# Optimization experiments

Measured on AMD Instinct MI355X. Metric: run time of the kernel, lower is better.

## Reference

```python
import jax, jax.numpy as jnp
import numpy as np

HEADS = 4
DIM_HEAD = 32
IN_CHANNELS = 256
SCALE = DIM_HEAD ** -0.5
EPS = 1e-5


def setup_inputs() -> dict:
    key = jax.random.key(0)
    ks = jax.random.split(key, 6)
    B, C, H, W = 16, IN_CHANNELS, 64, 64
    inner = HEADS * DIM_HEAD  # 128
    x = jax.random.normal(ks[0], (B, C, H, W), dtype=jnp.float32)
    # 1x1 conv weights are [out_ch, in_ch] (kernel spatial dims are 1)
    w_qkv = jax.random.normal(ks[1], (3 * inner, C), dtype=jnp.float32) * (C ** -0.5)
    w_out = jax.random.normal(ks[2], (C, inner), dtype=jnp.float32) * (inner ** -0.5)
    b_out = jax.random.normal(ks[3], (C,), dtype=jnp.float32) * 0.01
    gn_gamma = jnp.ones((C,), dtype=jnp.float32)
    gn_beta = jnp.zeros((C,), dtype=jnp.float32)
    return {"x": x, "w_qkv": w_qkv, "w_out": w_out, "b_out": b_out,
            "gn_gamma": gn_gamma, "gn_beta": gn_beta}


def reference(x, w_qkv, w_out, b_out, gn_gamma, gn_beta):
    b, c, h, w = x.shape
    n = h * w
    inner = HEADS * DIM_HEAD
    # 1x1 conv (no bias): [b, 3*inner, h, w], then chunk into q,k,v along channels
    qkv = jnp.einsum('oc,bchw->bohw', w_qkv, x)
    qkv = qkv.reshape(b, 3, HEADS, DIM_HEAD, n)  # chunk + 'b (h c) x y -> b h c (x y)'
    q, k, v = qkv[:, 0], qkv[:, 1], qkv[:, 2]    # each [b, heads, dim_head, n]
    q = jax.nn.softmax(q, axis=-2) * SCALE       # softmax over dim_head axis
    k = jax.nn.softmax(k, axis=-1)               # softmax over spatial axis
    context = jnp.einsum('bhdn,bhen->bhde', k, v)  # [b, heads, d, e]
    out = jnp.einsum('bhde,bhdn->bhen', context, q)  # [b, heads, e, n]
    out = out.reshape(b, inner, h, w)            # 'b h c (x y) -> b (h c) x y'
    # out 1x1 conv with bias
    out = jnp.einsum('oc,bchw->bohw', w_out, out) + b_out[None, :, None, None]
    # GroupNorm(num_groups=1): normalize over (C,H,W) per sample, per-channel affine
    mean = jnp.mean(out, axis=(1, 2, 3), keepdims=True)
    var = jnp.var(out, axis=(1, 2, 3), keepdims=True)
    out = (out - mean) * jax.lax.rsqrt(var + EPS)
    return out * gn_gamma[None, :, None, None] + gn_beta[None, :, None, None]
```

## Files before the change

kernel.cpp:

```cpp
#include <hip/hip_runtime.h>
#include <hip/hip_bf16.h>
#include <math.h>

#define B_SZ 16
#define C_IN 256
#define HEADS 4
#define DHEAD 32
#define INNER 128
#define QKV_CH 384
#define N_PIX 4096
#define SCALE_Q 0.17677669529663687f
#define GN_EPS 1e-5f
#define NCHK 32

typedef __attribute__((ext_vector_type(8))) short s16x8;
typedef __attribute__((ext_vector_type(4))) float f32x4;
typedef __attribute__((ext_vector_type(8))) unsigned short u16x8;
typedef __attribute__((ext_vector_type(4))) unsigned short u16x4;

#define VMCNT(n) asm volatile("s_waitcnt vmcnt(" #n ")" ::: "memory")
#define LGKMCNT0 asm volatile("s_waitcnt lgkmcnt(0)" ::: "memory")

__device__ __forceinline__ float waveSum(float v) {
#pragma unroll
  for (int off = 32; off > 0; off >>= 1) v += __shfl_down(v, off, 64);
  return v;
}
__device__ __forceinline__ unsigned short f2bf(float f) {
  unsigned int u = __builtin_bit_cast(unsigned int, f);
  unsigned int r = 0x7FFFu + ((u >> 16) & 1u);
  return (unsigned short)((u + r) >> 16);
}
__device__ __forceinline__ float bf2f(unsigned short u) {
  unsigned int x = ((unsigned int)u) << 16;
  return __builtin_bit_cast(float, x);
}

__global__ __launch_bounds__(256) void cvt_w(const float* __restrict__ wq,
                                             const float* __restrict__ wo,
                                             unsigned short* __restrict__ wqb,
                                             unsigned short* __restrict__ wob) {
  const int i = blockIdx.x * 256 + threadIdx.x;
  if (i < QKV_CH * C_IN) wqb[i] = f2bf(wq[i]);
  if (i < C_IN * INNER) wob[i] = f2bf(wo[i]);
}

__global__ __launch_bounds__(512, 4) void qkv_gemm(const unsigned short* __restrict__ A,
                                                   const float* __restrict__ X,
                                                   unsigned short* __restrict__ Out,
                                                   unsigned short* __restrict__ qsm_t) {
  const int b = blockIdx.y;
  const int n0 = blockIdx.x * 64;
  const int tid = threadIdx.x;
  const int w = tid >> 6, l = tid & 63;
  const int lr = l & 15, kg = l >> 4;
  const int wm = w >> 1, wn = w & 1;

  __shared__ char lds[65536];
  char* As = lds;
  char* Bs = lds + 49152;

  const int c_loc = ((tid >> 3) & 7) + w * 8;
  const int oct = tid & 7;
  const float* xbase = X + (size_t)b * C_IN * N_PIX + (size_t)c_loc * N_PIX + n0 + oct * 8;

  auto ISSUE_A = [&](int kc, int half) {
#pragma unroll
    for (int it = 0; it < 3; ++it) {
      const int idx = it * 512 + tid;
      const int r = idx >> 3;
      const int srcb = ((idx & 7) << 4) ^ ((r & 7) << 4);
      __builtin_amdgcn_global_load_lds(
          (const __attribute__((address_space(1))) void*)((const char*)A +
              ((size_t)(half * 192 + r) * C_IN + kc * 64) * 2 + srcb),
          (__attribute__((address_space(3))) void*)(As + half * 24576 + idx * 16), 16, 0, 0);
    }
  };

  f32x4 xr0, xr1;
  auto ISSUE_X = [&](int kc) {
    const float* xp = xbase + (size_t)(kc * 64) * N_PIX;
    xr0 = *reinterpret_cast<const f32x4*>(xp);
    xr1 = *reinterpret_cast<const f32x4*>(xp + 4);
  };

  auto WRITE_B = [&](int pb) {
#pragma unroll
    for (int j = 0; j < 8; ++j) {
      const int n = oct * 8 + j;
      const float v = (j < 4) ? xr0[j] : xr1[j - 4];
      *reinterpret_cast<unsigned short*>(
          Bs + pb * 8192 + n * 128 + ((2 * c_loc) ^ (((n ^ (n >> 3)) & 7) << 4))) = f2bf(v);
    }
  };

  f32x4 acc[2][3][2] = {};

  auto COMPUTE = [&](int kc, int half) {
    const char* Ab = As + half * 24576;
    const char* Bb = Bs + (kc & 1) * 8192;
#pragma unroll
    for (int ks = 0; ks < 2; ++ks) {
      const int kb = ks * 64 + kg * 16;
      s16x8 av[3], bv[2];
#pragma unroll
      for (int i = 0; i < 3; ++i) {
        const int r = wm * 48 + i * 16 + lr;
        av[i] = *reinterpret_cast<const s16x8*>(Ab + r * 128 + (kb ^ ((r & 7) << 4)));
      }
#pragma unroll
      for (int j = 0; j < 2; ++j) {
        const int n = wn * 32 + j * 16 + lr;
        bv[j] = *reinterpret_cast<const s16x8*>(Bb + n * 128 +
                                                (kb ^ (((n ^ (n >> 3)) & 7) << 4)));
      }
#pragma unroll
      for (int i = 0; i < 3; ++i)
#pragma unroll
        for (int j = 0; j < 2; ++j)
          acc[half][i][j] =
              __builtin_amdgcn_mfma_f32_16x16x32_bf16(av[i], bv[j], acc[half][i][j], 0, 0, 0);
    }
  };

  ISSUE_A(0, 0);
  ISSUE_X(0);
  VMCNT(0);
  WRITE_B(0);
  LGKMCNT0;
  __builtin_amdgcn_s_barrier();

  for (int kc = 0; kc < 4; ++kc) {
    ISSUE_A(kc, 1);
    if (kc < 3) {
      ISSUE_X(kc + 1);
      VMCNT(5);
    } else {
      VMCNT(3);
    }
    __builtin_amdgcn_s_barrier();
    COMPUTE(kc, 0);
    LGKMCNT0;
    __builtin_amdgcn_s_barrier();
    if (kc < 3) {
      ISSUE_A(kc + 1, 0);
      VMCNT(3);
    } else {
      VMCNT(0);
    }
    __builtin_amdgcn_s_barrier();
    if (kc < 3) WRITE_B((kc + 1) & 1);
    COMPUTE(kc, 1);
    LGKMCNT0;
    __builtin_amdgcn_s_barrier();
  }

  unsigned short* Ob = Out + (size_t)b * QKV_CH * N_PIX;
#pragma unroll
  for (int half = 0; half < 2; ++half)
#pragma unroll
    for (int i = 0; i < 3; ++i) {
      const int mt = wm * 48 + i * 16;
      if (half == 1 || mt >= 128) {
        const int mrow = half * 192 + mt + kg * 4;
#pragma unroll
        for (int j = 0; j < 2; ++j) {
          const int col = n0 + wn * 32 + j * 16 + lr;
#pragma unroll
          for (int r = 0; r < 4; ++r)
            Ob[(size_t)(mrow + r) * N_PIX + col] = f2bf(acc[half][i][j][r]);
        }
      }
    }

  float* qs = (float*)lds;
#pragma unroll
  for (int i = 0; i < 3; ++i) {
    const int mt = wm * 48 + i * 16;
    if (mt < 128) {
      const int rowb = mt + kg * 4;
#pragma unroll
      for (int j = 0; j < 2; ++j) {
        const int c_l = wn * 32 + j * 16 + lr;
        *reinterpret_cast<f32x4*>(qs + c_l * 132 + rowb) = acc[0][i][j];
      }
    }
  }
  LGKMCNT0;
  __builtin_amdgcn_s_barrier();

  if (tid < 256) {
    const int n_loc = tid & 63, h = tid >> 6;
    const float* qrow = qs + n_loc * 132 + h * 32;
    f32x4 qv[8];
#pragma unroll
    for (int c = 0; c < 8; ++c) qv[c] = *reinterpret_cast<const f32x4*>(qrow + c * 4);
    float m = qv[0][0];
#pragma unroll
    for (int c = 0; c < 8; ++c)
#pragma unroll
      for (int r = 0; r < 4; ++r) m = fmaxf(m, qv[c][r]);
    float e[32];
    float s = 0.f;
#pragma unroll
    for (int c = 0; c < 8; ++c)
#pragma unroll
      for (int r = 0; r < 4; ++r) {
        e[c * 4 + r] = __expf(qv[c][r] - m);
        s += e[c * 4 + r];
      }
    const float inv = SCALE_Q / s;
    unsigned short* ob = qsm_t + ((size_t)b * N_PIX + n0 + n_loc) * INNER + h * DHEAD;
#pragma unroll
    for (int d8 = 0; d8 < 4; ++d8) {
      u16x8 pk;
#pragma unroll
      for (int r = 0; r < 8; ++r) pk[r] = f2bf(e[d8 * 8 + r] * inv);
      *reinterpret_cast<u16x8*>(&ob[d8 * 8]) = pk;
    }
  }
}

__global__ __launch_bounds__(256) void ctx_mfma(const unsigned short* __restrict__ qkv,
                                                float* __restrict__ ctxp,
                                                float* __restrict__ mpart,
                                                float* __restrict__ spart) {
  const int id = blockIdx.x;
  const int rank = (id & 7) * 64 + (id >> 3);
  const int wid = rank * 4 + (threadIdx.x >> 6);
  const int l = threadIdx.x & 63;
  const int b = wid >> 7;
  const int h = (wid >> 5) & 3;
  const int c = wid & 31;
  const int lr = l & 15, kg = l >> 4;
  const unsigned short* kb =
      qkv + ((size_t)b * QKV_CH + INNER + h * DHEAD) * N_PIX + c * 128 + kg * 8;
  const unsigned short* vb = kb + (size_t)INNER * N_PIX;

  u16x8 kf[2][4], vf[2][4];
#pragma unroll
  for (int dt = 0; dt < 2; ++dt)
#pragma unroll
    for (int ks = 0; ks < 4; ++ks) {
      kf[dt][ks] = *reinterpret_cast<const u16x8*>(kb + (size_t)(dt * 16 + lr) * N_PIX + ks * 32);
      vf[dt][ks] = *reinterpret_cast<const u16x8*>(vb + (size_t)(dt * 16 + lr) * N_PIX + ks * 32);
    }
  float kv[2][4][8];
  float m[2] = {-INFINITY, -INFINITY};
#pragma unroll
  for (int dt = 0; dt < 2; ++dt)
#pragma unroll
    for (int ks = 0; ks < 4; ++ks)
#pragma unroll
      for (int j = 0; j < 8; ++j) {
        kv[dt][ks][j] = bf2f(kf[dt][ks][j]);
        m[dt] = fmaxf(m[dt], kv[dt][ks][j]);
      }
#pragma unroll
  for (int dt = 0; dt < 2; ++dt) {
    m[dt] = fmaxf(m[dt], __shfl_xor(m[dt], 16, 64));
    m[dt] = fmaxf(m[dt], __shfl_xor(m[dt], 32, 64));
  }
  float s[2] = {0.f, 0.f};
  s16x8 ka[2][4];
#pragma unroll
  for (int dt = 0; dt < 2; ++dt)
#pragma unroll
    for (int ks = 0; ks < 4; ++ks)
#pragma unroll
      for (int j = 0; j < 8; ++j) {
        const float e = __expf(kv[dt][ks][j] - m[dt]);
        s[dt] += e;
        ka[dt][ks][j] = (short)f2bf(e);
      }
#pragma unroll
  for (int dt = 0; dt < 2; ++dt) {
    s[dt] += __shfl_xor(s[dt], 16, 64);
    s[dt] += __shfl_xor(s[dt], 32, 64);
  }
  f32x4 acc[2][2] = {};
#pragma unroll
  for (int ks = 0; ks < 4; ++ks)
#pragma unroll
    for (int dt = 0; dt < 2; ++dt)
#pragma unroll
      for (int et = 0; et < 2; ++et)
        acc[dt][et] = __builtin_amdgcn_mfma_f32_16x16x32_bf16(
            ka[dt][ks], __builtin_bit_cast(s16x8, vf[et][ks]), acc[dt][et], 0, 0, 0);

  float* cp = ctxp + (size_t)wid * 1024;
#pragma unroll
  for (int dt = 0; dt < 2; ++dt)
#pragma unroll
    for (int et = 0; et < 2; ++et)
#pragma unroll
      for (int r = 0; r < 4; ++r)
        cp[(dt * 16 + kg * 4 + r) * 32 + et * 16 + lr] = acc[dt][et][r];
  if (kg == 0) {
    mpart[wid * 32 + lr] = m[0];
    mpart[wid * 32 + 16 + lr] = m[1];
    spart[wid * 32 + lr] = s[0];
    spart[wid * 32 + 16 + lr] = s[1];
  }
}

__global__ __launch_bounds__(256) void ctx_weff(const float* __restrict__ ctxp,
                                                const float* __restrict__ mpart,
                                                const float* __restrict__ spart,
                                                const unsigned short* __restrict__ wo,
                                                unsigned short* __restrict__ weff) {
  const int bh = blockIdx.x;
  const int b = bh >> 2, h = bh & 3;
  const int tid = threadIdx.x;
  __shared__ float ms[NCHK][32], ss[NCHK][32], fac[NCHK][32];
  __shared__ float inv_l[32];
  __shared__ float cf[1024];
#pragma unroll
  for (int i = 0; i < 4; ++i) {
    const int idx = tid + i * 256;
    ms[idx >> 5][idx & 31] = mpart[(size_t)bh * 1024 + idx];
    ss[idx >> 5][idx & 31] = spart[(size_t)bh * 1024 + idx];
  }
  __syncthreads();
  if (tid < 32) {
    const int d = tid;
    float M = -INFINITY;
#pragma unroll
    for (int c = 0; c < NCHK; ++c) M = fmaxf(M, ms[c][d]);
    float den = 0.f;
#pragma unroll
    for (int c = 0; c < NCHK; ++c) {
      const float f = __expf(ms[c][d] - M);
      fac[c][d] = f;
      den += f * ss[c][d];
    }
    inv_l[d] = 1.0f / den;
  }
  __syncthreads();
  const float* cp = ctxp + (size_t)bh * (NCHK * 1024);
  for (int i = 0; i < 4; ++i) {
    const int idx = tid + i * 256;
    const int d = idx >> 5;
    float vals[NCHK];
#pragma unroll
    for (int c = 0; c < NCHK; ++c) vals[c] = cp[(size_t)c * 1024 + idx];
    float a = 0.f;
#pragma unroll
    for (int c = 0; c < NCHK; ++c) a += fac[c][d] * vals[c];
    cf[idx] = a * inv_l[d];
  }
  __syncthreads();

  const int o = tid;
  float wr[32];
  const unsigned short* wp = wo + (size_t)o * INNER + h * DHEAD;
#pragma unroll
  for (int e8 = 0; e8 < 4; ++e8) {
    u16x8 v = *reinterpret_cast<const u16x8*>(wp + e8 * 8);
#pragma unroll
    for (int j = 0; j < 8; ++j) wr[e8 * 8 + j] = bf2f(v[j]);
  }
  unsigned short* op = weff + ((size_t)b * C_IN + o) * INNER + h * DHEAD;
#pragma unroll
  for (int d8 = 0; d8 < 4; ++d8) {
    u16x8 outv;
#pragma unroll
    for (int dd = 0; dd < 8; ++dd) {
      const float* cr = cf + (d8 * 8 + dd) * 32;
      float a = 0.f;
#pragma unroll
      for (int e4 = 0; e4 < 8; ++e4) {
        const f32x4 c4 = *reinterpret_cast<const f32x4*>(cr + e4 * 4);
#pragma unroll
        for (int j = 0; j < 4; ++j) a += wr[e4 * 4 + j] * c4[j];
      }
      outv[dd] = f2bf(a);
    }
    *reinterpret_cast<u16x8*>(op + d8 * 8) = outv;
  }
}

template <bool WRITE>
__global__ __launch_bounds__(256) void out_gemm_t(
    const unsigned short* __restrict__ A, const unsigned short* __restrict__ Bm,
    float* __restrict__ Out, const float* __restrict__ bias,
    float* __restrict__ gn_part, const float* __restrict__ gamma,
    const float* __restrict__ beta) {
  const int id = blockIdx.x;
  const int rank = (id & 7) * 128 + (id >> 3);
  const int b = rank >> 6;
  const int m0 = ((rank >> 5) & 1) * 128;
  const int n0 = (rank & 31) * 128;
  const int tid = threadIdx.x;
  const int w = tid >> 6, l = tid & 63;
  const int lr = l & 15, kg = l >> 4;
  const int mOff = (w >> 1) * 64, nOff = (w & 1) * 64;

  __shared__ unsigned short As[8192];
  __shared__ unsigned short Bs[8192];
  __shared__ float red[8];

  const unsigned short* Ab = A + (size_t)b * C_IN * INNER;
  const unsigned short* Bb = Bm + (size_t)b * N_PIX * INNER;
  f32x4 acc[4][4] = {};

  for (int kc = 0; kc < INNER; kc += 64) {
#pragma unroll
    for (int s = 0; s < 4; ++s) {
      const int blk = (w * 4 + s) * 64 + l;
      const int r = blk >> 3;
      const int c = ((blk & 7) ^ (r & 7)) << 3;
      __builtin_amdgcn_global_load_lds(
          (const __attribute__((address_space(1))) void*)(Ab + (size_t)(m0 + r) * INNER + kc + c),
          (__attribute__((address_space(3))) void*)((char*)As + (w * 4 + s) * 1024), 16, 0, 0);
      __builtin_amdgcn_global_load_lds(
          (const __attribute__((address_space(1))) void*)(Bb + (size_t)(n0 + r) * INNER + kc + c),
          (__attribute__((address_space(3))) void*)((char*)Bs + (w * 4 + s) * 1024), 16, 0, 0);
    }
    __syncthreads();
#pragma unroll
    for (int ks = 0; ks < 2; ++ks) {
      const int kbyte = ks * 64 + kg * 16;
      s16x8 av[4], bv[4];
#pragma unroll
      for (int i = 0; i < 4; ++i) {
        const int row = mOff + i * 16 + lr;
        av[i] = *reinterpret_cast<const s16x8*>(
            (const char*)As + row * 128 + (kbyte ^ ((row & 7) << 4)));
      }
#pragma unroll
      for (int j = 0; j < 4; ++j) {
        const int row = nOff + j * 16 + lr;
        bv[j] = *reinterpret_cast<const s16x8*>(
            (const char*)Bs + row * 128 + (kbyte ^ ((row & 7) << 4)));
      }
#pragma unroll
      for (int i = 0; i < 4; ++i)
#pragma unroll
        for (int j = 0; j < 4; ++j)
          acc[i][j] = __builtin_amdgcn_mfma_f32_16x16x32_bf16(av[i], bv[j], acc[i][j], 0, 0, 0);
    }
    __syncthreads();
  }

  if (!WRITE) {
    float s = 0.f, s2 = 0.f;
#pragma unroll
    for (int i = 0; i < 4; ++i) {
      const int rowb = m0 + mOff + i * 16 + kg * 4;
#pragma unroll
      for (int r = 0; r < 4; ++r) {
        const float bvs = bias[rowb + r];
#pragma unroll
        for (int j = 0; j < 4; ++j) {
          const float v = acc[i][j][r] + bvs;
          s += v;
          s2 += v * v;
        }
      }
    }
    const float S = waveSum(s), S2 = waveSum(s2);
    if (l == 0) {
      red[w] = S;
      red[4 + w] = S2;
    }
    __syncthreads();
    if (tid == 0) {
      gn_part[(size_t)rank * 2 + 0] = red[0] + red[1] + red[2] + red[3];
      gn_part[(size_t)rank * 2 + 1] = red[4] + red[5] + red[6] + red[7];
    }
  } else {
    const int i64 = tid & 63;
    float ps = gn_part[(size_t)(b * 64 + i64) * 2 + 0];
    float ps2 = gn_part[(size_t)(b * 64 + i64) * 2 + 1];
    ps = waveSum(ps);
    ps2 = waveSum(ps2);
    const float invn = 1.0f / (float)(C_IN * N_PIX);
    const float mean = __shfl(ps, 0, 64) * invn;
    const float var = __shfl(ps2, 0, 64) * invn - mean * mean;
    const float istd = rsqrtf(var + GN_EPS);

    float* Ob = Out + (size_t)b * C_IN * N_PIX;
#pragma unroll
    for (int i = 0; i < 4; ++i) {
      const int rowb = m0 + mOff + i * 16 + kg * 4;
#pragma unroll
      for (int r = 0; r < 4; ++r) {
        const int ch = rowb + r;
        const float bvs = bias[ch];
        const float g = gamma[ch] * istd;
        const float be = beta[ch];
#pragma unroll
        for (int j = 0; j < 4; ++j) {
          const int col = n0 + nOff + j * 16 + lr;
          const float v = acc[i][j][r] + bvs;
          Ob[(size_t)ch * N_PIX + col] = (v - mean) * g + be;
        }
      }
    }
  }
}

extern "C" void kernel_launch(void* const* d_in, const int* in_sizes, int n_in,
                              void* d_out, int out_size, void* d_ws, size_t ws_size,
                              hipStream_t stream) {
  const float* x = (const float*)d_in[0];
  const float* w_qkv = (const float*)d_in[1];
  const float* w_out = (const float*)d_in[2];
  const float* b_out = (const float*)d_in[3];
  const float* gamma = (const float*)d_in[4];
  const float* beta = (const float*)d_in[5];
  float* out = (float*)d_out;

  char* p = (char*)d_ws;
  unsigned short* qkv_bf = (unsigned short*)p; p += (size_t)B_SZ * QKV_CH * N_PIX * 2;
  unsigned short* qsm_t = (unsigned short*)p;  p += (size_t)B_SZ * N_PIX * INNER * 2;
  unsigned short* wq_bf = (unsigned short*)p;  p += (size_t)QKV_CH * C_IN * 2;
  unsigned short* wo_bf = (unsigned short*)p;  p += (size_t)C_IN * INNER * 2;
  float* ctxp = (float*)p;    p += (size_t)B_SZ * HEADS * NCHK * 1024 * 4;
  float* mpart = (float*)p;   p += (size_t)B_SZ * HEADS * NCHK * 32 * 4;
  float* spart = (float*)p;   p += (size_t)B_SZ * HEADS * NCHK * 32 * 4;
  unsigned short* weff = (unsigned short*)p; p += (size_t)B_SZ * C_IN * INNER * 2;
  float* gn_part = (float*)p; p += (size_t)1024 * 2 * 4;

  cvt_w<<<dim3(384), 256, 0, stream>>>(w_qkv, w_out, wq_bf, wo_bf);
  qkv_gemm<<<dim3(64, B_SZ), 512, 0, stream>>>(wq_bf, x, qkv_bf, qsm_t);
  ctx_mfma<<<dim3(512), 256, 0, stream>>>(qkv_bf, ctxp, mpart, spart);
  ctx_weff<<<dim3(64), 256, 0, stream>>>(ctxp, mpart, spart, wo_bf, weff);
  out_gemm_t<false><<<dim3(1024), 256, 0, stream>>>(
      weff, qsm_t, nullptr, b_out, gn_part, nullptr, nullptr);
  out_gemm_t<true><<<dim3(1024), 256, 0, stream>>>(
      weff, qsm_t, out, b_out, gn_part, gamma, beta);
}
```

Baseline: 82.73 us.

## Fuse two-pass output GEMM into one kernel with a grid-wide atomic barrier

The output GEMM used to run twice, once to gather GroupNorm partial sums and once to recompute and write the normalized output. It now runs once: each block publishes its partial sums, waits on a global atomic counter until all 1024 blocks arrive, then normalizes and writes straight from registers. This removes the duplicate GEMM and one launch. It relies on all 1024 blocks being resident at once (launch bounds 256,4). If they are not, the spin-wait only ends at its iteration cap, and the output is then wrong or slow.

```diff
diff --git a/kernel.cpp b/kernel.cpp
--- a/kernel.cpp
+++ b/kernel.cpp
@@ -39,8 +39,10 @@
 __global__ __launch_bounds__(256) void cvt_w(const float* __restrict__ wq,
                                              const float* __restrict__ wo,
                                              unsigned short* __restrict__ wqb,
-                                             unsigned short* __restrict__ wob) {
+                                             unsigned short* __restrict__ wob,
+                                             unsigned int* __restrict__ bar) {
   const int i = blockIdx.x * 256 + threadIdx.x;
+  if (i == 0) *bar = 0u;
   if (i < QKV_CH * C_IN) wqb[i] = f2bf(wq[i]);
   if (i < C_IN * INNER) wob[i] = f2bf(wo[i]);
 }
@@ -380,12 +382,11 @@
   }
 }
 
-template <bool WRITE>
-__global__ __launch_bounds__(256) void out_gemm_t(
+__global__ __launch_bounds__(256, 4) void out_full(
     const unsigned short* __restrict__ A, const unsigned short* __restrict__ Bm,
     float* __restrict__ Out, const float* __restrict__ bias,
     float* __restrict__ gn_part, const float* __restrict__ gamma,
-    const float* __restrict__ beta) {
+    const float* __restrict__ beta, unsigned int* __restrict__ bar) {
   const int id = blockIdx.x;
   const int rank = (id & 7) * 128 + (id >> 3);
   const int b = rank >> 6;
@@ -443,7 +444,7 @@
     __syncthreads();
   }
 
-  if (!WRITE) {
+  {
     float s = 0.f, s2 = 0.f;
 #pragma unroll
     for (int i = 0; i < 4; ++i) {
@@ -469,33 +470,44 @@
       gn_part[(size_t)rank * 2 + 0] = red[0] + red[1] + red[2] + red[3];
       gn_part[(size_t)rank * 2 + 1] = red[4] + red[5] + red[6] + red[7];
     }
-  } else {
-    const int i64 = tid & 63;
-    float ps = gn_part[(size_t)(b * 64 + i64) * 2 + 0];
-    float ps2 = gn_part[(size_t)(b * 64 + i64) * 2 + 1];
-    ps = waveSum(ps);
-    ps2 = waveSum(ps2);
-    const float invn = 1.0f / (float)(C_IN * N_PIX);
-    const float mean = __shfl(ps, 0, 64) * invn;
-    const float var = __shfl(ps2, 0, 64) * invn - mean * mean;
-    const float istd = rsqrtf(var + GN_EPS);
-
-    float* Ob = Out + (size_t)b * C_IN * N_PIX;
-#pragma unroll
-    for (int i = 0; i < 4; ++i) {
-      const int rowb = m0 + mOff + i * 16 + kg * 4;
-#pragma unroll
-      for (int r = 0; r < 4; ++r) {
-        const int ch = rowb + r;
-        const float bvs = bias[ch];
-        const float g = gamma[ch] * istd;
-        const float be = beta[ch];
-#pragma unroll
-        for (int j = 0; j < 4; ++j) {
-          const int col = n0 + nOff + j * 16 + lr;
-          const float v = acc[i][j][r] + bvs;
-          Ob[(size_t)ch * N_PIX + col] = (v - mean) * g + be;
-        }
+  }
+
+  __syncthreads();
+  if (tid == 0) {
+    __threadfence();
+    __hip_atomic_fetch_add(bar, 1u, __ATOMIC_ACQ_REL, __HIP_MEMORY_SCOPE_AGENT);
+    for (long t = 0; t < (1L << 24); ++t) {
+      if (__hip_atomic_load(bar, __ATOMIC_ACQUIRE, __HIP_MEMORY_SCOPE_AGENT) >= 1024u) break;
+      __builtin_amdgcn_s_sleep(8);
+    }
+  }
+  __syncthreads();
+
+  const int i64 = tid & 63;
+  float ps = gn_part[(size_t)(b * 64 + i64) * 2 + 0];
+  float ps2 = gn_part[(size_t)(b * 64 + i64) * 2 + 1];
+  ps = waveSum(ps);
+  ps2 = waveSum(ps2);
+  const float invn = 1.0f / (float)(C_IN * N_PIX);
+  const float mean = __shfl(ps, 0, 64) * invn;
+  const float var = __shfl(ps2, 0, 64) * invn - mean * mean;
+  const float istd = rsqrtf(var + GN_EPS);
+
+  float* Ob = Out + (size_t)b * C_IN * N_PIX;
+#pragma unroll
+  for (int i = 0; i < 4; ++i) {
+    const int rowb = m0 + mOff + i * 16 + kg * 4;
+#pragma unroll
+    for (int r = 0; r < 4; ++r) {
+      const int ch = rowb + r;
+      const float bvs = bias[ch];
+      const float g = gamma[ch] * istd;
+      const float be = beta[ch];
+#pragma unroll
+      for (int j = 0; j < 4; ++j) {
+        const int col = n0 + nOff + j * 16 + lr;
+        const float v = acc[i][j][r] + bvs;
+        Ob[(size_t)ch * N_PIX + col] = (v - mean) * g + be;
       }
     }
   }
@@ -522,13 +534,12 @@
   float* spart = (float*)p;   p += (size_t)B_SZ * HEADS * NCHK * 32 * 4;
   unsigned short* weff = (unsigned short*)p; p += (size_t)B_SZ * C_IN * INNER * 2;
   float* gn_part = (float*)p; p += (size_t)1024 * 2 * 4;
-
-  cvt_w<<<dim3(384), 256, 0, stream>>>(w_qkv, w_out, wq_bf, wo_bf);
+  unsigned int* bar = (unsigned int*)p; p += 128;
+
+  cvt_w<<<dim3(384), 256, 0, stream>>>(w_qkv, w_out, wq_bf, wo_bf, bar);
   qkv_gemm<<<dim3(64, B_SZ), 512, 0, stream>>>(wq_bf, x, qkv_bf, qsm_t);
   ctx_mfma<<<dim3(512), 256, 0, stream>>>(qkv_bf, ctxp, mpart, spart);
   ctx_weff<<<dim3(64), 256, 0, stream>>>(ctxp, mpart, spart, wo_bf, weff);
-  out_gemm_t<false><<<dim3(1024), 256, 0, stream>>>(
-      weff, qsm_t, nullptr, b_out, gn_part, nullptr, nullptr);
-  out_gemm_t<true><<<dim3(1024), 256, 0, stream>>>(
-      weff, qsm_t, out, b_out, gn_part, gamma, beta);
-}
+  out_full<<<dim3(1024), 256, 0, stream>>>(
+      weff, qsm_t, out, b_out, gn_part, gamma, beta, bar);
+}
```

Result: slower. 148.2 us (+79.2%).

## Fuse k-softmax context computation into QKV GEMM epilogue, drop qkv buffer

Applied to the files above, without the earlier changes.

The QKV GEMM epilogue now stages q, k and v tiles as bf16 in LDS. Each block computes q-softmax and also per-chunk k-softmax partials and the k·v^T context via MFMA, producing 64 chunks per (batch, head) instead of 32. This removes the separate ctx_mfma kernel and the full bf16 qkv round-trip through global memory. In exchange the GEMM epilogue does more work, q is now rounded to bf16 before its softmax, and the ctx_weff reduction has twice as many partials to combine.

```diff
diff --git a/kernel.cpp b/kernel.cpp
--- a/kernel.cpp
+++ b/kernel.cpp
@@ -11,7 +11,10 @@
 #define N_PIX 4096
 #define SCALE_Q 0.17677669529663687f
 #define GN_EPS 1e-5f
-#define NCHK 32
+#define NCHK 64
+
+#define KOFF 16896
+#define VOFF 34304
 
 typedef __attribute__((ext_vector_type(8))) short s16x8;
 typedef __attribute__((ext_vector_type(4))) float f32x4;
@@ -47,8 +50,10 @@
 
 __global__ __launch_bounds__(512, 4) void qkv_gemm(const unsigned short* __restrict__ A,
                                                    const float* __restrict__ X,
-                                                   unsigned short* __restrict__ Out,
-                                                   unsigned short* __restrict__ qsm_t) {
+                                                   unsigned short* __restrict__ qsm_t,
+                                                   float* __restrict__ ctxp,
+                                                   float* __restrict__ mpart,
+                                                   float* __restrict__ spart) {
   const int b = blockIdx.y;
   const int n0 = blockIdx.x * 64;
   const int tid = threadIdx.x;
@@ -155,152 +160,138 @@
     __builtin_amdgcn_s_barrier();
   }
 
-  unsigned short* Ob = Out + (size_t)b * QKV_CH * N_PIX;
 #pragma unroll
   for (int half = 0; half < 2; ++half)
 #pragma unroll
-    for (int i = 0; i < 3; ++i) {
-      const int mt = wm * 48 + i * 16;
-      if (half == 1 || mt >= 128) {
-        const int mrow = half * 192 + mt + kg * 4;
-#pragma unroll
-        for (int j = 0; j < 2; ++j) {
-          const int col = n0 + wn * 32 + j * 16 + lr;
+    for (int i = 0; i < 3; ++i)
+#pragma unroll
+      for (int j = 0; j < 2; ++j) {
+        const int chb = half * 192 + wm * 48 + i * 16 + kg * 4;
+        const int col = wn * 32 + j * 16 + lr;
+        u16x4 pk;
+#pragma unroll
+        for (int r = 0; r < 4; ++r) pk[r] = f2bf(acc[half][i][j][r]);
+        if (chb < 128) {
+          *reinterpret_cast<u16x4*>(lds + col * 264 + chb * 2) = pk;
+        } else if (chb < 256) {
 #pragma unroll
           for (int r = 0; r < 4; ++r)
-            Ob[(size_t)(mrow + r) * N_PIX + col] = f2bf(acc[half][i][j][r]);
+            *reinterpret_cast<unsigned short*>(lds + KOFF + (chb - 128 + r) * 136 + col * 2) =
+                pk[r];
+        } else {
+#pragma unroll
+          for (int r = 0; r < 4; ++r)
+            *reinterpret_cast<unsigned short*>(lds + VOFF + (chb - 256 + r) * 136 + col * 2) =
+                pk[r];
         }
       }
-    }
-
-  float* qs = (float*)lds;
-#pragma unroll
-  for (int i = 0; i < 3; ++i) {
-    const int mt = wm * 48 + i * 16;
-    if (mt < 128) {
-      const int rowb = mt + kg * 4;
-#pragma unroll
-      for (int j = 0; j < 2; ++j) {
-        const int c_l = wn * 32 + j * 16 + lr;
-        *reinterpret_cast<f32x4*>(qs + c_l * 132 + rowb) = acc[0][i][j];
-      }
-    }
-  }
   LGKMCNT0;
   __builtin_amdgcn_s_barrier();
 
   if (tid < 256) {
-    const int n_loc = tid & 63, h = tid >> 6;
-    const float* qrow = qs + n_loc * 132 + h * 32;
-    f32x4 qv[8];
-#pragma unroll
-    for (int c = 0; c < 8; ++c) qv[c] = *reinterpret_cast<const f32x4*>(qrow + c * 4);
-    float m = qv[0][0];
-#pragma unroll
-    for (int c = 0; c < 8; ++c)
-#pragma unroll
-      for (int r = 0; r < 4; ++r) m = fmaxf(m, qv[c][r]);
-    float e[32];
+    const int n_loc = tid & 63, h2 = tid >> 6;
+    float q[32];
+#pragma unroll
+    for (int c = 0; c < 8; ++c) {
+      u16x4 v4 = *reinterpret_cast<const u16x4*>(lds + n_loc * 264 + h2 * 64 + c * 8);
+#pragma unroll
+      for (int t = 0; t < 4; ++t) q[c * 4 + t] = bf2f(v4[t]);
+    }
+    float m = q[0];
+#pragma unroll
+    for (int t = 1; t < 32; ++t) m = fmaxf(m, q[t]);
     float s = 0.f;
 #pragma unroll
-    for (int c = 0; c < 8; ++c)
-#pragma unroll
-      for (int r = 0; r < 4; ++r) {
-        e[c * 4 + r] = __expf(qv[c][r] - m);
-        s += e[c * 4 + r];
-      }
+    for (int t = 0; t < 32; ++t) {
+      q[t] = __expf(q[t] - m);
+      s += q[t];
+    }
     const float inv = SCALE_Q / s;
-    unsigned short* ob = qsm_t + ((size_t)b * N_PIX + n0 + n_loc) * INNER + h * DHEAD;
+    unsigned short* ob = qsm_t + ((size_t)b * N_PIX + n0 + n_loc) * INNER + h2 * DHEAD;
 #pragma unroll
     for (int d8 = 0; d8 < 4; ++d8) {
       u16x8 pk;
 #pragma unroll
-      for (int r = 0; r < 8; ++r) pk[r] = f2bf(e[d8 * 8 + r] * inv);
+      for (int r = 0; r < 8; ++r) pk[r] = f2bf(q[d8 * 8 + r] * inv);
       *reinterpret_cast<u16x8*>(&ob[d8 * 8]) = pk;
     }
   }
-}
-
-__global__ __launch_bounds__(256) void ctx_mfma(const unsigned short* __restrict__ qkv,
-                                                float* __restrict__ ctxp,
-                                                float* __restrict__ mpart,
-                                                float* __restrict__ spart) {
-  const int id = blockIdx.x;
-  const int rank = (id & 7) * 64 + (id >> 3);
-  const int wid = rank * 4 + (threadIdx.x >> 6);
-  const int l = threadIdx.x & 63;
-  const int b = wid >> 7;
-  const int h = (wid >> 5) & 3;
-  const int c = wid & 31;
-  const int lr = l & 15, kg = l >> 4;
-  const unsigned short* kb =
-      qkv + ((size_t)b * QKV_CH + INNER + h * DHEAD) * N_PIX + c * 128 + kg * 8;
-  const unsigned short* vb = kb + (size_t)INNER * N_PIX;
-
-  u16x8 kf[2][4], vf[2][4];
-#pragma unroll
-  for (int dt = 0; dt < 2; ++dt)
-#pragma unroll
-    for (int ks = 0; ks < 4; ++ks) {
-      kf[dt][ks] = *reinterpret_cast<const u16x8*>(kb + (size_t)(dt * 16 + lr) * N_PIX + ks * 32);
-      vf[dt][ks] = *reinterpret_cast<const u16x8*>(vb + (size_t)(dt * 16 + lr) * N_PIX + ks * 32);
-    }
-  float kv[2][4][8];
-  float m[2] = {-INFINITY, -INFINITY};
-#pragma unroll
-  for (int dt = 0; dt < 2; ++dt)
-#pragma unroll
-    for (int ks = 0; ks < 4; ++ks)
-#pragma unroll
-      for (int j = 0; j < 8; ++j) {
-        kv[dt][ks][j] = bf2f(kf[dt][ks][j]);
-        m[dt] = fmaxf(m[dt], kv[dt][ks][j]);
-      }
-#pragma unroll
-  for (int dt = 0; dt < 2; ++dt) {
-    m[dt] = fmaxf(m[dt], __shfl_xor(m[dt], 16, 64));
-    m[dt] = fmaxf(m[dt], __shfl_xor(m[dt], 32, 64));
-  }
-  float s[2] = {0.f, 0.f};
-  s16x8 ka[2][4];
-#pragma unroll
-  for (int dt = 0; dt < 2; ++dt)
-#pragma unroll
-    for (int ks = 0; ks < 4; ++ks)
-#pragma unroll
-      for (int j = 0; j < 8; ++j) {
-        const float e = __expf(kv[dt][ks][j] - m[dt]);
-        s[dt] += e;
-        ka[dt][ks][j] = (short)f2bf(e);
-      }
-#pragma unroll
-  for (int dt = 0; dt < 2; ++dt) {
-    s[dt] += __shfl_xor(s[dt], 16, 64);
-    s[dt] += __shfl_xor(s[dt], 32, 64);
-  }
-  f32x4 acc[2][2] = {};
-#pragma unroll
-  for (int ks = 0; ks < 4; ++ks)
+
+  {
+    const int h = w >> 1, et = w & 1;
+    float kvv[2][2][8];
 #pragma unroll
     for (int dt = 0; dt < 2; ++dt)
 #pragma unroll
-      for (int et = 0; et < 2; ++et)
-        acc[dt][et] = __builtin_amdgcn_mfma_f32_16x16x32_bf16(
-            ka[dt][ks], __builtin_bit_cast(s16x8, vf[et][ks]), acc[dt][et], 0, 0, 0);
-
-  float* cp = ctxp + (size_t)wid * 1024;
-#pragma unroll
-  for (int dt = 0; dt < 2; ++dt)
-#pragma unroll
-    for (int et = 0; et < 2; ++et)
+      for (int ks = 0; ks < 2; ++ks) {
+        const char* base = lds + KOFF + (h * 32 + dt * 16 + lr) * 136 + (ks * 32 + kg * 8) * 2;
+        u16x4 lo = *reinterpret_cast<const u16x4*>(base);
+        u16x4 hi = *reinterpret_cast<const u16x4*>(base + 8);
+#pragma unroll
+        for (int t = 0; t < 4; ++t) {
+          kvv[dt][ks][t] = bf2f(lo[t]);
+          kvv[dt][ks][4 + t] = bf2f(hi[t]);
+        }
+      }
+    float m2[2] = {-INFINITY, -INFINITY};
+#pragma unroll
+    for (int dt = 0; dt < 2; ++dt) {
+#pragma unroll
+      for (int ks = 0; ks < 2; ++ks)
+#pragma unroll
+        for (int t = 0; t < 8; ++t) m2[dt] = fmaxf(m2[dt], kvv[dt][ks][t]);
+      m2[dt] = fmaxf(m2[dt], __shfl_xor(m2[dt], 16, 64));
+      m2[dt] = fmaxf(m2[dt], __shfl_xor(m2[dt], 32, 64));
+    }
+    float s2[2] = {0.f, 0.f};
+    s16x8 ka[2][2];
+#pragma unroll
+    for (int dt = 0; dt < 2; ++dt) {
+#pragma unroll
+      for (int ks = 0; ks < 2; ++ks)
+#pragma unroll
+        for (int t = 0; t < 8; ++t) {
+          const float ev = __expf(kvv[dt][ks][t] - m2[dt]);
+          s2[dt] += ev;
+          ka[dt][ks][t] = (short)f2bf(ev);
+        }
+      s2[dt] += __shfl_xor(s2[dt], 16, 64);
+      s2[dt] += __shfl_xor(s2[dt], 32, 64);
+    }
+    s16x8 vfrag[2];
+#pragma unroll
+    for (int ks = 0; ks < 2; ++ks) {
+      const char* base = lds + VOFF + (h * 32 + et * 16 + lr) * 136 + (ks * 32 + kg * 8) * 2;
+      u16x4 lo = *reinterpret_cast<const u16x4*>(base);
+      u16x4 hi = *reinterpret_cast<const u16x4*>(base + 8);
+      u16x8 vv;
+#pragma unroll
+      for (int t = 0; t < 4; ++t) {
+        vv[t] = lo[t];
+        vv[4 + t] = hi[t];
+      }
+      vfrag[ks] = __builtin_bit_cast(s16x8, vv);
+    }
+    f32x4 accc[2] = {};
+#pragma unroll
+    for (int ks = 0; ks < 2; ++ks)
+#pragma unroll
+      for (int dt = 0; dt < 2; ++dt)
+        accc[dt] = __builtin_amdgcn_mfma_f32_16x16x32_bf16(ka[dt][ks], vfrag[ks], accc[dt], 0, 0, 0);
+
+    const size_t wid = ((size_t)(b * HEADS + h)) * NCHK + blockIdx.x;
+    float* cp = ctxp + wid * 1024;
+#pragma unroll
+    for (int dt = 0; dt < 2; ++dt)
 #pragma unroll
       for (int r = 0; r < 4; ++r)
-        cp[(dt * 16 + kg * 4 + r) * 32 + et * 16 + lr] = acc[dt][et][r];
-  if (kg == 0) {
-    mpart[wid * 32 + lr] = m[0];
-    mpart[wid * 32 + 16 + lr] = m[1];
-    spart[wid * 32 + lr] = s[0];
-    spart[wid * 32 + 16 + lr] = s[1];
+        cp[(dt * 16 + kg * 4 + r) * 32 + et * 16 + lr] = accc[dt][r];
+    if (et == 0 && kg == 0) {
+      mpart[wid * 32 + lr] = m2[0];
+      mpart[wid * 32 + 16 + lr] = m2[1];
+      spart[wid * 32 + lr] = s2[0];
+      spart[wid * 32 + 16 + lr] = s2[1];
+    }
   }
 }
 
@@ -316,10 +307,10 @@
   __shared__ float inv_l[32];
   __shared__ float cf[1024];
 #pragma unroll
-  for (int i = 0; i < 4; ++i) {
+  for (int i = 0; i < 8; ++i) {
     const int idx = tid + i * 256;
-    ms[idx >> 5][idx & 31] = mpart[(size_t)bh * 1024 + idx];
-    ss[idx >> 5][idx & 31] = spart[(size_t)bh * 1024 + idx];
+    ms[idx >> 5][idx & 31] = mpart[(size_t)bh * 2048 + idx];
+    ss[idx >> 5][idx & 31] = spart[(size_t)bh * 2048 + idx];
   }
   __syncthreads();
   if (tid < 32) {
@@ -341,12 +332,15 @@
   for (int i = 0; i < 4; ++i) {
     const int idx = tid + i * 256;
     const int d = idx >> 5;
-    float vals[NCHK];
-#pragma unroll
-    for (int c = 0; c < NCHK; ++c) vals[c] = cp[(size_t)c * 1024 + idx];
     float a = 0.f;
 #pragma unroll
-    for (int c = 0; c < NCHK; ++c) a += fac[c][d] * vals[c];
+    for (int g = 0; g < 2; ++g) {
+      float vals[32];
+#pragma unroll
+      for (int c = 0; c < 32; ++c) vals[c] = cp[(size_t)(g * 32 + c) * 1024 + idx];
+#pragma unroll
+      for (int c = 0; c < 32; ++c) a += fac[g * 32 + c][d] * vals[c];
+    }
     cf[idx] = a * inv_l[d];
   }
   __syncthreads();
@@ -513,10 +507,9 @@
   float* out = (float*)d_out;
 
   char* p = (char*)d_ws;
-  unsigned short* qkv_bf = (unsigned short*)p; p += (size_t)B_SZ * QKV_CH * N_PIX * 2;
-  unsigned short* qsm_t = (unsigned short*)p;  p += (size_t)B_SZ * N_PIX * INNER * 2;
-  unsigned short* wq_bf = (unsigned short*)p;  p += (size_t)QKV_CH * C_IN * 2;
-  unsigned short* wo_bf = (unsigned short*)p;  p += (size_t)C_IN * INNER * 2;
+  unsigned short* qsm_t = (unsigned short*)p; p += (size_t)B_SZ * N_PIX * INNER * 2;
+  unsigned short* wq_bf = (unsigned short*)p; p += (size_t)QKV_CH * C_IN * 2;
+  unsigned short* wo_bf = (unsigned short*)p; p += (size_t)C_IN * INNER * 2;
   float* ctxp = (float*)p;    p += (size_t)B_SZ * HEADS * NCHK * 1024 * 4;
   float* mpart = (float*)p;   p += (size_t)B_SZ * HEADS * NCHK * 32 * 4;
   float* spart = (float*)p;   p += (size_t)B_SZ * HEADS * NCHK * 32 * 4;
@@ -524,8 +517,7 @@
   float* gn_part = (float*)p; p += (size_t)1024 * 2 * 4;
 
   cvt_w<<<dim3(384), 256, 0, stream>>>(w_qkv, w_out, wq_bf, wo_bf);
-  qkv_gemm<<<dim3(64, B_SZ), 512, 0, stream>>>(wq_bf, x, qkv_bf, qsm_t);
-  ctx_mfma<<<dim3(512), 256, 0, stream>>>(qkv_bf, ctxp, mpart, spart);
+  qkv_gemm<<<dim3(64, B_SZ), 512, 0, stream>>>(wq_bf, x, qsm_t, ctxp, mpart, spart);
   ctx_weff<<<dim3(64), 256, 0, stream>>>(ctxp, mpart, spart, wo_bf, weff);
   out_gemm_t<false><<<dim3(1024), 256, 0, stream>>>(
       weff, qsm_t, nullptr, b_out, gn_part, nullptr, nullptr);
```

Result: faster. 79.88 us (median of 3 runs) (-3.4%).
